# Optimization experiments

Measured on AMD Instinct MI355X. Metric: run time of the kernel, lower is better.

The kernel has to match this reference:

```python
import jax, jax.numpy as jnp
import numpy as np

B, H, W, D = 128, 128, 512, 10000
P_BERNOULLI = 0.5


def setup_inputs() -> dict:
    key = jax.random.key(0)
    kx, kw = jax.random.split(key)
    x = jax.random.normal(kx, (B, H, W), dtype=jnp.float32)
    # random +/-1 projection: 2*Bernoulli(p) - 1
    bern = (jax.random.uniform(kw, (W, D)) < P_BERNOULLI).astype(jnp.float32)
    hdweights = 2.0 * bern - 1.0
    return {"x": x, "hdweights": hdweights}


def reference(x, hdweights):
    # Original: sign(sum_h(x @ Wh)). Matmul is linear, so the sum over the
    # channel axis h commutes with the projection; einsum contracts both at
    # once without materializing the (B, h, D) intermediate.
    out = jnp.einsum("bhw,wd->bd", x, hdweights)  # == sum over h of (x @ W)
    return jnp.sign(out)
```

## Files before the change

### kernel.cpp

```cpp
#include <hip/hip_runtime.h>
#include <stdint.h>

constexpr int Dn = 10000;
constexpr int Bn = 128;
constexpr int Wn = 512;
constexpr int Hn = 128;
constexpr int NTILES = 157;

typedef float  f32x4  __attribute__((ext_vector_type(4)));
typedef short  bf16x8 __attribute__((ext_vector_type(8)));

__device__ inline uint16_t f32_to_bf16(float f) {
    uint32_t u = __builtin_bit_cast(uint32_t, f);
    return (uint16_t)((u + 0x7FFFu + ((u >> 16) & 1u)) >> 16);
}
__device__ inline float bf16_to_f32(uint16_t h) {
    uint32_t u = ((uint32_t)h) << 16;
    return __builtin_bit_cast(float, u);
}

__global__ __launch_bounds__(256) void prep(const float* __restrict__ x,
                                            const float* __restrict__ wts,
                                            double* __restrict__ sT64,
                                            uint16_t* __restrict__ aHi,
                                            uint16_t* __restrict__ aLo,
                                            uint32_t* __restrict__ bitsT) {
    int bid = blockIdx.x;
    if (bid < 512) {
        int b  = bid >> 2;
        int w0 = (bid & 3) << 7;
        int wc = threadIdx.x & 31;
        int hs = threadIdx.x >> 5;
        const f32x4* p = (const f32x4*)(x + (size_t)b * (Hn * Wn)
                                          + (size_t)(hs * 16) * Wn + w0) + wc;
        double a0 = 0, a1 = 0, a2 = 0, a3 = 0;
        #pragma unroll
        for (int h = 0; h < 16; ++h) {
            f32x4 f = p[(size_t)h * (Wn / 4)];
            a0 += (double)f.x; a1 += (double)f.y;
            a2 += (double)f.z; a3 += (double)f.w;
        }
        __shared__ double red[8][128];
        red[hs][wc * 4 + 0] = a0;
        red[hs][wc * 4 + 1] = a1;
        red[hs][wc * 4 + 2] = a2;
        red[hs][wc * 4 + 3] = a3;
        __syncthreads();
        if (threadIdx.x < 128) {
            int wl = threadIdx.x;
            double s = 0.0;
            #pragma unroll
            for (int k = 0; k < 8; ++k) s += red[k][wl];
            int w = w0 + wl;
            sT64[(size_t)b * Wn + w] = s;
            float s32 = (float)s;
            uint16_t hi = f32_to_bf16(s32);
            float hif = bf16_to_f32(hi);
            uint16_t lo = f32_to_bf16(s32 - hif);
            int ktile = w >> 5;
            int mtile = b >> 4;
            int lane  = (b & 15) | (((w >> 3) & 3) << 4);
            int j     = w & 7;
            size_t idx = (size_t)((ktile * 8 + mtile) * 64 + lane) * 8 + j;
            aHi[idx] = hi;
            aLo[idx] = lo;
        }
    } else {
        int idx = (bid - 512) * 256 + (int)threadIdx.x;
        int g = idx / Dn;
        int d = idx - g * Dn;
        uint32_t m = 0;
        #pragma unroll
        for (int j = 0; j < 32; ++j)
            m |= (wts[(size_t)(g * 32 + j) * Dn + d] > 0.0f) ? (1u << j) : 0u;
        bitsT[(size_t)d * 16 + g] = m;
    }
}

__global__ __launch_bounds__(256) void gemm_mfma(const uint32_t* __restrict__ bitsT,
                                                 const uint16_t* __restrict__ aHi,
                                                 const uint16_t* __restrict__ aLo,
                                                 const double* __restrict__ sT64,
                                                 float* __restrict__ out) {
    __shared__ uint4 shA[2048];
    int tid  = (int)threadIdx.x;
    int lane = tid & 63;
    int wid  = tid >> 6;
    int mt   = blockIdx.y;

    const uint4* AhU = (const uint4*)aHi;
    const uint4* AlU = (const uint4*)aLo;
    #pragma unroll
    for (int c = 0; c < 8; ++c) {
        int e = tid + 256 * c;
        int chunk = e >> 6;
        int l = e & 63;
        int g = chunk & 15;
        const uint4* src = (chunk < 16 ? AhU : AlU) + (size_t)(g * 8 + mt) * 64 + l;
        shA[e] = *src;
    }

    int t = blockIdx.x * 4 + wid;
    if (t >= NTILES) t = NTILES - 1;
    int ln = lane & 15;
    int lh = lane >> 4;
    int sh = lh * 8;
    int dbase = t * 64;

    uint32_t wrd[4][16];
    #pragma unroll
    for (int nt = 0; nt < 4; ++nt) {
        int d = dbase + nt * 16 + ln;
        int dc = d < Dn ? d : Dn - 1;
        const uint4* wp = (const uint4*)(bitsT + (size_t)dc * 16);
        #pragma unroll
        for (int q = 0; q < 4; ++q) {
            uint4 v = wp[q];
            wrd[nt][4 * q + 0] = v.x; wrd[nt][4 * q + 1] = v.y;
            wrd[nt][4 * q + 2] = v.z; wrd[nt][4 * q + 3] = v.w;
        }
    }

    __syncthreads();

    f32x4 acc[4];
    #pragma unroll
    for (int nt = 0; nt < 4; ++nt) acc[nt] = (f32x4){0.f, 0.f, 0.f, 0.f};

    const bf16x8* shAv = (const bf16x8*)shA;
    #pragma unroll
    for (int g = 0; g < 16; ++g) {
        bf16x8 ah = shAv[g * 64 + lane];
        bf16x8 al = shAv[(16 + g) * 64 + lane];
        #pragma unroll
        for (int nt = 0; nt < 4; ++nt) {
            uint32_t t8 = (wrd[nt][g] >> sh) & 0xFFu;
            int bw0 = (int)(0xBF80BF80u ^ (((t8 & 1u) << 15) | ((t8 & 2u) << 30)));
            int bw1 = (int)(0xBF80BF80u ^ ((((t8 >> 2) & 1u) << 15) | (((t8 >> 3) & 1u) << 31)));
            int bw2 = (int)(0xBF80BF80u ^ ((((t8 >> 4) & 1u) << 15) | (((t8 >> 5) & 1u) << 31)));
            int bw3 = (int)(0xBF80BF80u ^ ((((t8 >> 6) & 1u) << 15) | (((t8 >> 7) & 1u) << 31)));
            union { int i[4]; bf16x8 v; } bu;
            bu.i[0] = bw0; bu.i[1] = bw1; bu.i[2] = bw2; bu.i[3] = bw3;
            bf16x8 bf = bu.v;
            acc[nt] = __builtin_amdgcn_mfma_f32_16x16x32_bf16(ah, bf, acc[nt], 0, 0, 0);
            acc[nt] = __builtin_amdgcn_mfma_f32_16x16x32_bf16(al, bf, acc[nt], 0, 0, 0);
        }
    }

    #pragma unroll
    for (int nt = 0; nt < 4; ++nt) {
        int d = dbase + nt * 16 + ln;
        bool valid = d < Dn;
        #pragma unroll
        for (int r = 0; r < 4; ++r) {
            int b = mt * 16 + lh * 4 + r;
            float v = acc[nt][r];
            if (valid) out[(size_t)b * Dn + d] = v > 0.0f ? 1.0f : -1.0f;
            unsigned long long mask = __ballot(valid && fabsf(v) <= 0.25f);
            while (mask) {
                int l = __ffsll((long long)mask) - 1;
                mask &= mask - 1;
                int bl = mt * 16 + (l >> 4) * 4 + r;
                int dl = dbase + nt * 16 + (l & 15);
                const double* srow = sT64 + (size_t)bl * Wn;
                double a = 0.0;
                #pragma unroll
                for (int k = 0; k < 8; ++k) {
                    int w = lane + 64 * k;
                    uint32_t mw = bitsT[(size_t)dl * 16 + (w >> 5)];
                    double s = srow[w];
                    a += ((mw >> (w & 31)) & 1u) ? s : -s;
                }
                #pragma unroll
                for (int off = 32; off >= 1; off >>= 1)
                    a += __shfl_xor(a, off, 64);
                if (lane == l)
                    out[(size_t)bl * Dn + dl] = (a > 0.0) ? 1.0f : ((a < 0.0) ? -1.0f : 0.0f);
            }
        }
    }
}

extern "C" void kernel_launch(void* const* d_in, const int* in_sizes, int n_in,
                              void* d_out, int out_size, void* d_ws, size_t ws_size,
                              hipStream_t stream) {
    const float* x   = (const float*)d_in[0];
    const float* wts = (const float*)d_in[1];
    float* out = (float*)d_out;
    char* ws = (char*)d_ws;

    double*   sT64  = (double*)(ws);
    uint16_t* aHi   = (uint16_t*)(ws + 524288);
    uint16_t* aLo   = (uint16_t*)(ws + 655360);
    uint32_t* bitsT = (uint32_t*)(ws + 786432);

    prep<<<1137, 256, 0, stream>>>(x, wts, sT64, aHi, aLo, bitsT);
    gemm_mfma<<<dim3(40, 8), 256, 0, stream>>>(bitsT, aHi, aLo, sT64, out);
}
```

Before: 28.05 us.

## Precompute bf16 ±1 B-fragments in prep and use one N-tile per wave

The prep kernel now also writes the ±1 weights as bf16 values already laid out in MFMA fragment order (about 10 MB extra). The GEMM loads these fragments straight from memory instead of rebuilding them from bitmasks with per-element bit manipulation. Each wave now handles one 16-column tile instead of four, and the grid grows from 40x8 to 157x8 blocks to raise parallelism. The cost is extra global write and read traffic for the expanded weights, and more redundant loads of the A tiles into shared memory across the larger grid.

```diff
diff --git a/kernel.cpp b/kernel.cpp
--- a/kernel.cpp
+++ b/kernel.cpp
@@ -6,6 +6,7 @@
 constexpr int Wn = 512;
 constexpr int Hn = 128;
 constexpr int NTILES = 157;
+constexpr int NTD = 625;
 
 typedef float  f32x4  __attribute__((ext_vector_type(4)));
 typedef short  bf16x8 __attribute__((ext_vector_type(8)));
@@ -24,7 +25,8 @@
                                             double* __restrict__ sT64,
                                             uint16_t* __restrict__ aHi,
                                             uint16_t* __restrict__ aLo,
-                                            uint32_t* __restrict__ bitsT) {
+                                            uint32_t* __restrict__ bitsT,
+                                            uint16_t* __restrict__ bF) {
     int bid = blockIdx.x;
     if (bid < 512) {
         int b  = bid >> 2;
@@ -70,23 +72,42 @@
         int g = idx / Dn;
         int d = idx - g * Dn;
         uint32_t m = 0;
+        uint32_t pk[16];
         #pragma unroll
-        for (int j = 0; j < 32; ++j)
-            m |= (wts[(size_t)(g * 32 + j) * Dn + d] > 0.0f) ? (1u << j) : 0u;
+        for (int q = 0; q < 4; ++q) {
+            #pragma unroll
+            for (int jp = 0; jp < 4; ++jp) {
+                int w = g * 32 + q * 8 + jp * 2;
+                uint32_t v0 = (wts[(size_t)w * Dn + d]       > 0.0f) ? 0x3F80u : 0xBF80u;
+                uint32_t v1 = (wts[(size_t)(w + 1) * Dn + d] > 0.0f) ? 0x3F80u : 0xBF80u;
+                pk[q * 4 + jp] = v0 | (v1 << 16);
+                m |= (v0 == 0x3F80u ? 1u : 0u) << (q * 8 + jp * 2);
+                m |= (v1 == 0x3F80u ? 1u : 0u) << (q * 8 + jp * 2 + 1);
+            }
+        }
         bitsT[(size_t)d * 16 + g] = m;
+        int td = d >> 4;
+        uint4* dst = (uint4*)(bF + (size_t)(g * NTD + td) * 512 + ((d & 15) << 3));
+        #pragma unroll
+        for (int q = 0; q < 4; ++q) {
+            uint4 u; u.x = pk[q*4+0]; u.y = pk[q*4+1]; u.z = pk[q*4+2]; u.w = pk[q*4+3];
+            dst[q * 16] = u;
+        }
     }
 }
 
-__global__ __launch_bounds__(256) void gemm_mfma(const uint32_t* __restrict__ bitsT,
-                                                 const uint16_t* __restrict__ aHi,
-                                                 const uint16_t* __restrict__ aLo,
-                                                 const double* __restrict__ sT64,
-                                                 float* __restrict__ out) {
+__global__ __launch_bounds__(256, 4) void gemm_mfma(const uint16_t* __restrict__ bF,
+                                                    const uint16_t* __restrict__ aHi,
+                                                    const uint16_t* __restrict__ aLo,
+                                                    const uint32_t* __restrict__ bitsT,
+                                                    const double* __restrict__ sT64,
+                                                    float* __restrict__ out) {
     __shared__ uint4 shA[2048];
     int tid  = (int)threadIdx.x;
     int lane = tid & 63;
     int wid  = tid >> 6;
     int mt   = blockIdx.y;
+    int t    = blockIdx.x;
 
     const uint4* AhU = (const uint4*)aHi;
     const uint4* AlU = (const uint4*)aLo;
@@ -100,83 +121,55 @@
         shA[e] = *src;
     }
 
-    int t = blockIdx.x * 4 + wid;
-    if (t >= NTILES) t = NTILES - 1;
-    int ln = lane & 15;
-    int lh = lane >> 4;
-    int sh = lh * 8;
-    int dbase = t * 64;
-
-    uint32_t wrd[4][16];
+    int td = t * 4 + wid;
+    int tdc = td < NTD ? td : NTD - 1;
+    const bf16x8* BF = (const bf16x8*)bF;
+    bf16x8 bfr[16];
     #pragma unroll
-    for (int nt = 0; nt < 4; ++nt) {
-        int d = dbase + nt * 16 + ln;
-        int dc = d < Dn ? d : Dn - 1;
-        const uint4* wp = (const uint4*)(bitsT + (size_t)dc * 16);
-        #pragma unroll
-        for (int q = 0; q < 4; ++q) {
-            uint4 v = wp[q];
-            wrd[nt][4 * q + 0] = v.x; wrd[nt][4 * q + 1] = v.y;
-            wrd[nt][4 * q + 2] = v.z; wrd[nt][4 * q + 3] = v.w;
-        }
-    }
+    for (int g = 0; g < 16; ++g)
+        bfr[g] = BF[(size_t)(g * NTD + tdc) * 64 + lane];
 
     __syncthreads();
 
-    f32x4 acc[4];
-    #pragma unroll
-    for (int nt = 0; nt < 4; ++nt) acc[nt] = (f32x4){0.f, 0.f, 0.f, 0.f};
-
+    f32x4 acc = (f32x4){0.f, 0.f, 0.f, 0.f};
     const bf16x8* shAv = (const bf16x8*)shA;
     #pragma unroll
     for (int g = 0; g < 16; ++g) {
         bf16x8 ah = shAv[g * 64 + lane];
         bf16x8 al = shAv[(16 + g) * 64 + lane];
-        #pragma unroll
-        for (int nt = 0; nt < 4; ++nt) {
-            uint32_t t8 = (wrd[nt][g] >> sh) & 0xFFu;
-            int bw0 = (int)(0xBF80BF80u ^ (((t8 & 1u) << 15) | ((t8 & 2u) << 30)));
-            int bw1 = (int)(0xBF80BF80u ^ ((((t8 >> 2) & 1u) << 15) | (((t8 >> 3) & 1u) << 31)));
-            int bw2 = (int)(0xBF80BF80u ^ ((((t8 >> 4) & 1u) << 15) | (((t8 >> 5) & 1u) << 31)));
-            int bw3 = (int)(0xBF80BF80u ^ ((((t8 >> 6) & 1u) << 15) | (((t8 >> 7) & 1u) << 31)));
-            union { int i[4]; bf16x8 v; } bu;
-            bu.i[0] = bw0; bu.i[1] = bw1; bu.i[2] = bw2; bu.i[3] = bw3;
-            bf16x8 bf = bu.v;
-            acc[nt] = __builtin_amdgcn_mfma_f32_16x16x32_bf16(ah, bf, acc[nt], 0, 0, 0);
-            acc[nt] = __builtin_amdgcn_mfma_f32_16x16x32_bf16(al, bf, acc[nt], 0, 0, 0);
-        }
+        acc = __builtin_amdgcn_mfma_f32_16x16x32_bf16(ah, bfr[g], acc, 0, 0, 0);
+        acc = __builtin_amdgcn_mfma_f32_16x16x32_bf16(al, bfr[g], acc, 0, 0, 0);
     }
 
+    int ln = lane & 15;
+    int lh = lane >> 4;
+    int d = t * 64 + wid * 16 + ln;
+    bool valid = d < Dn;
     #pragma unroll
-    for (int nt = 0; nt < 4; ++nt) {
-        int d = dbase + nt * 16 + ln;
-        bool valid = d < Dn;
-        #pragma unroll
-        for (int r = 0; r < 4; ++r) {
-            int b = mt * 16 + lh * 4 + r;
-            float v = acc[nt][r];
-            if (valid) out[(size_t)b * Dn + d] = v > 0.0f ? 1.0f : -1.0f;
-            unsigned long long mask = __ballot(valid && fabsf(v) <= 0.25f);
-            while (mask) {
-                int l = __ffsll((long long)mask) - 1;
-                mask &= mask - 1;
-                int bl = mt * 16 + (l >> 4) * 4 + r;
-                int dl = dbase + nt * 16 + (l & 15);
-                const double* srow = sT64 + (size_t)bl * Wn;
-                double a = 0.0;
-                #pragma unroll
-                for (int k = 0; k < 8; ++k) {
-                    int w = lane + 64 * k;
-                    uint32_t mw = bitsT[(size_t)dl * 16 + (w >> 5)];
-                    double s = srow[w];
-                    a += ((mw >> (w & 31)) & 1u) ? s : -s;
-                }
-                #pragma unroll
-                for (int off = 32; off >= 1; off >>= 1)
-                    a += __shfl_xor(a, off, 64);
-                if (lane == l)
-                    out[(size_t)bl * Dn + dl] = (a > 0.0) ? 1.0f : ((a < 0.0) ? -1.0f : 0.0f);
+    for (int r = 0; r < 4; ++r) {
+        int b = mt * 16 + lh * 4 + r;
+        float v = acc[r];
+        if (valid) out[(size_t)b * Dn + d] = v > 0.0f ? 1.0f : -1.0f;
+        unsigned long long mask = __ballot(valid && fabsf(v) <= 0.25f);
+        while (mask) {
+            int l = __ffsll((long long)mask) - 1;
+            mask &= mask - 1;
+            int bl = mt * 16 + (l >> 4) * 4 + r;
+            int dl = t * 64 + wid * 16 + (l & 15);
+            const double* srow = sT64 + (size_t)bl * Wn;
+            double a = 0.0;
+            #pragma unroll
+            for (int k = 0; k < 8; ++k) {
+                int w = lane + 64 * k;
+                uint32_t mw = bitsT[(size_t)dl * 16 + (w >> 5)];
+                double s = srow[w];
+                a += ((mw >> (w & 31)) & 1u) ? s : -s;
             }
+            #pragma unroll
+            for (int off = 32; off >= 1; off >>= 1)
+                a += __shfl_xor(a, off, 64);
+            if (lane == l)
+                out[(size_t)bl * Dn + dl] = (a > 0.0) ? 1.0f : ((a < 0.0) ? -1.0f : 0.0f);
         }
     }
 }
@@ -193,7 +186,8 @@
     uint16_t* aHi   = (uint16_t*)(ws + 524288);
     uint16_t* aLo   = (uint16_t*)(ws + 655360);
     uint32_t* bitsT = (uint32_t*)(ws + 786432);
+    uint16_t* bF    = (uint16_t*)(ws + 1426432);
 
-    prep<<<1137, 256, 0, stream>>>(x, wts, sT64, aHi, aLo, bitsT);
-    gemm_mfma<<<dim3(40, 8), 256, 0, stream>>>(bitsT, aHi, aLo, sT64, out);
+    prep<<<1137, 256, 0, stream>>>(x, wts, sT64, aHi, aLo, bitsT, bF);
+    gemm_mfma<<<dim3(157, 8), 256, 0, stream>>>(bF, aHi, aLo, bitsT, sT64, out);
 }
```

Measured after the change: 33.72 us. 1.2x slower.
